# Kernel optimization log

Hardware: AMD Instinct MI355X
Metric: run time of the kernel (lower is better)

## Reference

```python
import jax, jax.numpy as jnp
import numpy as np

D = 1024
B, S = 4, 4096


def setup_inputs() -> dict:
    key = jax.random.key(0)
    ks = jax.random.split(key, 5)
    scale = 1.0 / np.sqrt(D)  # ~ torch Linear init magnitude
    return {
        "x": jax.random.normal(ks[0], (B, S, D), dtype=jnp.float32),
        "Wa": jax.random.normal(ks[1], (D, D), dtype=jnp.float32) * scale,
        "Wb": jax.random.normal(ks[2], (D, D), dtype=jnp.float32) * scale,
        "Wc": jax.random.normal(ks[3], (D, D), dtype=jnp.float32) * scale,
        "Wd": jax.random.normal(ks[4], (D, D), dtype=jnp.float32) * scale,
    }


def reference(x, Wa, Wb, Wc, Wd):
    # torch nn.Linear(bias=False): y = x @ W.T, W is [out, in]
    A = jax.nn.relu(jnp.einsum("bsd,ed->bse", x, Wa))
    Bm = jax.nn.relu(jnp.einsum("bsd,ed->bse", x, Wb))
    C = jax.nn.relu(jnp.einsum("bsd,ed->bse", x, Wc))
    cmp_matrix = jnp.einsum("bse,bte->bst", A, Bm)  # [B,S,S] unnormalized scores
    out = jnp.einsum("bst,bte->bse", cmp_matrix, C)
    return jax.nn.relu(jnp.einsum("bsd,ed->bse", out, Wd))
```

## Files before the change

### kernel.cpp

```cpp
#include <hip/hip_runtime.h>
#include <hip/hip_bf16.h>

#define D_ 1024
#define B_ 4
#define S_ 4096

typedef __attribute__((ext_vector_type(8))) short bf16x8;
typedef __attribute__((ext_vector_type(4))) float f32x4;
typedef __attribute__((ext_vector_type(4))) unsigned int u32x4;
typedef __attribute__((ext_vector_type(4))) unsigned short u16x4;

__device__ __forceinline__ unsigned short f2bf(float f) {
    unsigned int u = __builtin_bit_cast(unsigned int, f);
    u = u + 0x7fffu + ((u >> 16) & 1u);
    return (unsigned short)(u >> 16);
}
__device__ __forceinline__ unsigned int pk2(float a, float b) {
    return (unsigned int)f2bf(a) | ((unsigned int)f2bf(b) << 16);
}
__device__ __forceinline__ float bf2f(unsigned short h) {
    unsigned int u = ((unsigned int)h) << 16;
    return __builtin_bit_cast(float, u);
}
__device__ __forceinline__ void gload16(const void* g, void* l) {
    __builtin_amdgcn_global_load_lds(
        (const __attribute__((address_space(1))) void*)g,
        (__attribute__((address_space(3))) void*)l, 16, 0, 0);
}

__global__ __launch_bounds__(256)
void conv_bf16(const float* __restrict__ src, unsigned short* __restrict__ dst, int n8) {
    int i = blockIdx.x * blockDim.x + threadIdx.x;
    const int stride = gridDim.x * blockDim.x;
    for (; i < n8; i += stride) {
        f32x4 v0 = *(const f32x4*)(src + (size_t)i * 8);
        f32x4 v1 = *(const f32x4*)(src + (size_t)i * 8 + 4);
        u32x4 o;
        o[0] = pk2(v0[0], v0[1]);
        o[1] = pk2(v0[2], v0[3]);
        o[2] = pk2(v1[0], v1[1]);
        o[3] = pk2(v1[2], v1[3]);
        *(u32x4*)(dst + (size_t)i * 8) = o;
    }
}

__global__ __launch_bounds__(256)
void conv_bf16_w4(const float* __restrict__ s0, const float* __restrict__ s1,
                  const float* __restrict__ s2, const float* __restrict__ s3,
                  unsigned short* __restrict__ d0, unsigned short* __restrict__ d1,
                  unsigned short* __restrict__ d2, unsigned short* __restrict__ d3,
                  int n8_per) {
    int i = blockIdx.x * blockDim.x + threadIdx.x;
    const int stride = gridDim.x * blockDim.x;
    for (; i < 4 * n8_per; i += stride) {
        int w = i / n8_per;
        size_t j = (size_t)(i - w * n8_per) * 8;
        const float* s = (w == 0) ? s0 : (w == 1) ? s1 : (w == 2) ? s2 : s3;
        unsigned short* d = (w == 0) ? d0 : (w == 1) ? d1 : (w == 2) ? d2 : d3;
        f32x4 v0 = *(const f32x4*)(s + j);
        f32x4 v1 = *(const f32x4*)(s + j + 4);
        u32x4 o;
        o[0] = pk2(v0[0], v0[1]);
        o[1] = pk2(v0[2], v0[3]);
        o[2] = pk2(v1[0], v1[1]);
        o[3] = pk2(v1[2], v1[3]);
        *(u32x4*)(d + j) = o;
    }
}

__global__ __launch_bounds__(256)
void reduceN_bf16(const unsigned short* __restrict__ P, unsigned short* __restrict__ E,
                  int split, int n8_total) {
    int t = blockIdx.x * blockDim.x + threadIdx.x;
    const int stride = gridDim.x * blockDim.x;
    const int DD = D_ * D_;
    for (; t < n8_total; t += stride) {
        size_t idx = (size_t)t * 8;
        int b = (int)(idx / DD);
        size_t i = idx % DD;
        float s[8];
#pragma unroll
        for (int k = 0; k < 8; ++k) s[k] = 0.f;
        for (int seg = 0; seg < split; ++seg) {
            const unsigned short* p = P + (size_t)(b * split + seg) * DD + i;
            u16x4 v0 = *(const u16x4*)p;
            u16x4 v1 = *(const u16x4*)(p + 4);
#pragma unroll
            for (int k = 0; k < 4; ++k) { s[k] += bf2f(v0[k]); s[4 + k] += bf2f(v1[k]); }
        }
        u16x4 o0, o1;
#pragma unroll
        for (int k = 0; k < 4; ++k) { o0[k] = f2bf(s[k]); o1[k] = f2bf(s[4 + k]); }
        *(u16x4*)(E + idx) = o0;
        *(u16x4*)(E + idx + 4) = o1;
    }
}

#define BM 128
#define BN 128
#define BK 64
#define NTHR 256

template<bool OUT_F32, bool TRANS, bool RELU>
__global__ __launch_bounds__(NTHR)
void gemm_nt(const unsigned short* __restrict__ Ap, const unsigned short* __restrict__ Bp,
             void* __restrict__ Op, int M, int N, int K, int klen, int split,
             long long sA, long long sB, long long sO)
{
    __shared__ char lds_a[BM * BK * 2];
    __shared__ char lds_b[BN * BK * 2];

    const int tid   = threadIdx.x;
    const int bz    = blockIdx.z;
    const int batch = bz / split;
    const int k0    = (bz % split) * klen;
    const int bm    = blockIdx.y * BM;
    const int bn    = blockIdx.x * BN;

    const unsigned short* Abase = Ap + (size_t)batch * sA + (size_t)bm * K;
    const unsigned short* Bbase = Bp + (size_t)batch * sB + (size_t)bn * K;

    const int lane = tid & 63;
    const int wave = tid >> 6;
    const int wm   = (wave >> 1) * 64;
    const int wn   = (wave & 1) * 64;
    const int l16  = lane & 15;
    const int lhi  = lane >> 4;

    const int srow0 = wave * 32 + (lane >> 3);
    const int schnk = (lane & 7) ^ (lane >> 3);
    const char* gA0 = (const char*)(Abase + (size_t)srow0 * K) + schnk * 16;
    const char* gB0 = (const char*)(Bbase + (size_t)srow0 * K) + schnk * 16;
    char* lA0 = lds_a + wave * 4096;
    char* lB0 = lds_b + wave * 4096;

    f32x4 acc[4][4];
#pragma unroll
    for (int i = 0; i < 4; ++i)
#pragma unroll
        for (int j = 0; j < 4; ++j)
            acc[i][j] = (f32x4){0.f, 0.f, 0.f, 0.f};

    for (int kt = k0; kt < k0 + klen; kt += BK) {
#pragma unroll
        for (int p = 0; p < 4; ++p)
            gload16(gA0 + ((size_t)p * 8 * K + kt) * 2, lA0 + p * 1024);
#pragma unroll
        for (int p = 0; p < 4; ++p)
            gload16(gB0 + ((size_t)p * 8 * K + kt) * 2, lB0 + p * 1024);
        __syncthreads();
#pragma unroll
        for (int kk = 0; kk < BK / 32; ++kk) {
            bf16x8 af[4], bfr[4];
#pragma unroll
            for (int i = 0; i < 4; ++i) {
                int row = wm + i * 16 + l16;
                int byt = (row * 128 + kk * 64 + lhi * 16) ^ ((row & 7) << 4);
                af[i] = *(const bf16x8*)(lds_a + byt);
            }
#pragma unroll
            for (int j = 0; j < 4; ++j) {
                int row = wn + j * 16 + l16;
                int byt = (row * 128 + kk * 64 + lhi * 16) ^ ((row & 7) << 4);
                bfr[j] = *(const bf16x8*)(lds_b + byt);
            }
#pragma unroll
            for (int i = 0; i < 4; ++i)
#pragma unroll
                for (int j = 0; j < 4; ++j)
                    acc[i][j] = __builtin_amdgcn_mfma_f32_16x16x32_bf16(af[i], bfr[j], acc[i][j], 0, 0, 0);
        }
        __syncthreads();
    }

    const size_t obase = (size_t)bz * (size_t)sO;
    if constexpr (!TRANS) {
#pragma unroll
        for (int i = 0; i < 4; ++i) {
            const int m0 = bm + wm + i * 16 + lhi * 4;
#pragma unroll
            for (int j = 0; j < 4; ++j) {
                const int n = bn + wn + j * 16 + l16;
#pragma unroll
                for (int r = 0; r < 4; ++r) {
                    float v = acc[i][j][r];
                    if constexpr (RELU) v = fmaxf(v, 0.f);
                    size_t addr = obase + (size_t)(m0 + r) * N + n;
                    if constexpr (OUT_F32) ((float*)Op)[addr] = v;
                    else ((unsigned short*)Op)[addr] = f2bf(v);
                }
            }
        }
    } else {
#pragma unroll
        for (int i = 0; i < 4; ++i) {
            const int m0 = bm + wm + i * 16 + lhi * 4;
#pragma unroll
            for (int j = 0; j < 4; ++j) {
                const int n = bn + wn + j * 16 + l16;
                u16x4 h;
#pragma unroll
                for (int r = 0; r < 4; ++r) {
                    float v = acc[i][j][r];
                    if constexpr (RELU) v = fmaxf(v, 0.f);
                    h[r] = f2bf(v);
                }
                *(u16x4*)((unsigned short*)Op + obase + (size_t)n * M + m0) = h;
            }
        }
    }
}

#define CTILE 65536
#define CBOFF 32768

template<bool OUT_F32, bool TRANS, bool RELU>
__global__ __launch_bounds__(512, 2)
void gemm256(const unsigned short* __restrict__ Ap, const unsigned short* __restrict__ Bp,
             void* __restrict__ Op, int M, int N, int K, int klen, int split,
             long long sA, long long sB, long long sO)
{
    __shared__ char lds[131072];
    const int tid  = threadIdx.x;
    const int wave = tid >> 6;
    const int lane = tid & 63;

    const int gx = gridDim.x, gy = gridDim.y;
    const int f   = blockIdx.x + gx * (blockIdx.y + gy * blockIdx.z);
    const int nwg = gx * gy * (int)gridDim.z;
    const int s   = (f & 7) * (nwg >> 3) + (f >> 3);
    const int lx  = s % gx;
    const int lyz = s / gx;
    const int ly  = lyz % gy;
    const int lz  = lyz / gy;

    const int batch = lz / split;
    const int k0    = (lz % split) * klen;
    const int bm    = ly * 256;
    const int bn    = lx * 256;

    const int wm  = (wave >> 2) * 128;
    const int wn  = (wave & 3) * 64;
    const int l16 = lane & 15, lhi = lane >> 4;

    const unsigned short* Abase = Ap + (size_t)batch * sA + (size_t)bm * K;
    const unsigned short* Bbase = Bp + (size_t)batch * sB + (size_t)bn * K;
    const int srow  = lane >> 3;
    const int schnk = (lane & 7) ^ srow;
    const size_t K2 = (size_t)K * 2;
    const char* gA = (const char*)Abase + (size_t)srow * K2 + (size_t)schnk * 16 + (size_t)k0 * 2;
    const char* gB = (const char*)Bbase + (size_t)srow * K2 + (size_t)schnk * 16 + (size_t)k0 * 2;

    f32x4 acc[8][4];
#pragma unroll
    for (int i = 0; i < 8; ++i)
#pragma unroll
        for (int j = 0; j < 4; ++j)
            acc[i][j] = (f32x4){0.f, 0.f, 0.f, 0.f};

    bf16x8 a[4][2], b0[2][2], b1[2][2];

    auto stageA = [&](int c, int t) {
#pragma unroll
        for (int h = 0; h < 2; ++h)
#pragma unroll
            for (int p = 0; p < 2; ++p)
                gload16(gA + (size_t)t * 128 + (size_t)(h * 128 + wave * 16 + p * 8) * K2,
                        lds + c * CTILE + h * 16384 + wave * 2048 + p * 1024);
    };
    auto stageB = [&](int c, int t) {
#pragma unroll
        for (int h = 0; h < 2; ++h)
#pragma unroll
            for (int p = 0; p < 2; ++p)
                gload16(gB + (size_t)t * 128 + (size_t)(h * 128 + wave * 16 + p * 8) * K2,
                        lds + c * CTILE + CBOFF + h * 16384 + wave * 2048 + p * 1024);
    };
    auto ldA = [&](int c, int mh) {
#pragma unroll
        for (int i4 = 0; i4 < 4; ++i4)
#pragma unroll
            for (int kk = 0; kk < 2; ++kk) {
                int row = wm + mh * 64 + i4 * 16 + l16;
                int byt = (row * 128 + kk * 64 + lhi * 16) ^ ((row & 7) << 4);
                a[i4][kk] = *(const bf16x8*)(lds + c * CTILE + byt);
            }
    };
    auto ldB = [&](int c, int nh, bf16x8 (&bb)[2][2]) {
#pragma unroll
        for (int j2 = 0; j2 < 2; ++j2)
#pragma unroll
            for (int kk = 0; kk < 2; ++kk) {
                int row = wn + nh * 32 + j2 * 16 + l16;
                int byt = (row * 128 + kk * 64 + lhi * 16) ^ ((row & 7) << 4);
                bb[j2][kk] = *(const bf16x8*)(lds + c * CTILE + CBOFF + byt);
            }
    };
    auto mm = [&](int mh, int nh, bf16x8 (&bb)[2][2]) {
        __builtin_amdgcn_s_setprio(1);
#pragma unroll
        for (int i4 = 0; i4 < 4; ++i4)
#pragma unroll
            for (int j2 = 0; j2 < 2; ++j2)
#pragma unroll
                for (int kk = 0; kk < 2; ++kk)
                    acc[mh * 4 + i4][nh * 2 + j2] = __builtin_amdgcn_mfma_f32_16x16x32_bf16(
                        a[i4][kk], bb[j2][kk], acc[mh * 4 + i4][nh * 2 + j2], 0, 0, 0);
        __builtin_amdgcn_s_setprio(0);
    };

#define BAR()  __builtin_amdgcn_s_barrier()
#define LGKM0() asm volatile("s_waitcnt lgkmcnt(0)" ::: "memory")
#define VM4()  asm volatile("s_waitcnt vmcnt(4)" ::: "memory")

    const int NT = klen / 64;
    stageA(0, 0); stageB(0, 0); stageA(1, 1);
    VM4();
    BAR();

    for (int itr = 0; itr < NT / 2; ++itr) {
        const int t1  = 2 * itr + 1;
        const int tp0 = (2 * itr + 2) % NT;
        const int tp1 = (2 * itr + 3) % NT;
        ldA(0, 0); ldB(0, 0, b0); stageB(1, t1);
        BAR(); LGKM0(); mm(0, 0, b0); BAR();
        ldB(0, 1, b1);
        BAR(); LGKM0(); mm(0, 1, b1); BAR();
        ldA(0, 1);
        BAR(); LGKM0(); mm(1, 0, b0); BAR();
        stageA(0, tp0);
        BAR(); mm(1, 1, b1); VM4(); BAR();
        ldA(1, 0); ldB(1, 0, b0); stageB(0, tp0);
        BAR(); LGKM0(); mm(0, 0, b0); BAR();
        ldB(1, 1, b1);
        BAR(); LGKM0(); mm(0, 1, b1); BAR();
        ldA(1, 1);
        BAR(); LGKM0(); mm(1, 0, b0); BAR();
        stageA(1, tp1);
        BAR(); mm(1, 1, b1); VM4(); BAR();
    }
    asm volatile("s_waitcnt vmcnt(0)" ::: "memory");

    const size_t obase = (size_t)lz * (size_t)sO;
    if constexpr (!TRANS) {
#pragma unroll
        for (int i = 0; i < 8; ++i) {
            const int m0 = bm + wm + i * 16 + lhi * 4;
#pragma unroll
            for (int j = 0; j < 4; ++j) {
                const int n = bn + wn + j * 16 + l16;
#pragma unroll
                for (int r = 0; r < 4; ++r) {
                    float v = acc[i][j][r];
                    if constexpr (RELU) v = fmaxf(v, 0.f);
                    size_t addr = obase + (size_t)(m0 + r) * N + n;
                    if constexpr (OUT_F32) ((float*)Op)[addr] = v;
                    else ((unsigned short*)Op)[addr] = f2bf(v);
                }
            }
        }
    } else {
#pragma unroll
        for (int i = 0; i < 8; ++i) {
            const int m0 = bm + wm + i * 16 + lhi * 4;
#pragma unroll
            for (int j = 0; j < 4; ++j) {
                const int n = bn + wn + j * 16 + l16;
                u16x4 h;
#pragma unroll
                for (int r = 0; r < 4; ++r) {
                    float v = acc[i][j][r];
                    if constexpr (RELU) v = fmaxf(v, 0.f);
                    h[r] = f2bf(v);
                }
                *(u16x4*)((unsigned short*)Op + obase + (size_t)n * M + m0) = h;
            }
        }
    }
#undef BAR
#undef LGKM0
#undef VM4
}

extern "C" void kernel_launch(void* const* d_in, const int* in_sizes, int n_in,
                              void* d_out, int out_size, void* d_ws, size_t ws_size,
                              hipStream_t stream) {
    (void)in_sizes; (void)n_in; (void)out_size;
    const float* x  = (const float*)d_in[0];
    const float* Wa = (const float*)d_in[1];
    const float* Wb = (const float*)d_in[2];
    const float* Wc = (const float*)d_in[3];
    const float* Wd = (const float*)d_in[4];

    const long long SD  = (long long)S_ * D_;
    const long long DD2 = (long long)D_ * D_;
    const size_t MB = 1024 * 1024;

    unsigned short* r0 = (unsigned short*)d_ws;
    unsigned short* r1 = (unsigned short*)((char*)d_ws + 32 * MB);
    unsigned short* Ft = r1;
    const bool big_ws = ws_size >= (size_t)96 * MB;

    char* ob = (char*)d_out;
    unsigned short* xb    = (unsigned short*)ob;
    unsigned short* Pp    = big_ws ? (unsigned short*)((char*)d_ws + 64 * MB)
                                   : (unsigned short*)(ob + 32 * MB);
    unsigned short* Enorm = (unsigned short*)(ob + 48 * MB);
    unsigned short* Wbb   = (unsigned short*)(ob + 56 * MB);
    unsigned short* Wcb   = (unsigned short*)(ob + 58 * MB);
    unsigned short* Wab   = (unsigned short*)(ob + 60 * MB);
    unsigned short* Wdb   = (unsigned short*)(ob + 62 * MB);
    const int esplit = big_ws ? 4 : 2;
    const int eklen  = S_ / esplit;

    dim3 blk256(256, 1, 1);
    dim3 blk512(512, 1, 1);
    dim3 gS(D_ / 256, S_ / 256, B_);
    dim3 gE(D_ / 256, D_ / 256, B_ * esplit);
    dim3 gF(D_ / BN, D_ / BM, B_);

    conv_bf16<<<2048, blk256, 0, stream>>>(x, xb, (B_ * S_ * D_) / 8);
    conv_bf16_w4<<<1024, blk256, 0, stream>>>(Wb, Wc, Wa, Wd, Wbb, Wcb, Wab, Wdb, (D_ * D_) / 8);

    gemm256<false, true,  true ><<<gS, blk512, 0, stream>>>(xb, Wbb, r0, S_, D_, D_, D_, 1, SD, 0, SD);
    gemm256<false, true,  true ><<<gS, blk512, 0, stream>>>(xb, Wcb, r1, S_, D_, D_, D_, 1, SD, 0, SD);
    gemm256<false, false, false><<<gE, blk512, 0, stream>>>(r0, r1, Pp, D_, D_, S_, eklen, esplit, SD, SD, DD2);
    reduceN_bf16<<<2048, blk256, 0, stream>>>(Pp, Enorm, esplit, (B_ * D_ * D_) / 8);
    gemm_nt<false, true,  false><<<gF, blk256, 0, stream>>>(Enorm, Wdb, Ft, D_, D_, D_, D_, 1, DD2, 0, DD2);
    gemm256<false, false, true ><<<gS, blk512, 0, stream>>>(xb, Wab, r0, S_, D_, D_, D_, 1, SD, 0, SD);
    gemm256<true,  false, true ><<<gS, blk512, 0, stream>>>(r0, Ft, (float*)d_out, S_, D_, D_, D_, 1, SD, DD2, SD);
}
```

Before: 250.5 us.

## Fuse B/C projections into one GEMM, reduce in place, simplify gemm256 pipeline

The two x@Wb and x@Wc projections become one N=2048 GEMM writing an interleaved buffer. The Gram product reads strided halves of that buffer. The split-K reduction now writes in place over the first partial, and the weight conversions are split and reordered so the out/workspace buffers can be reused. The gemm256 main loop drops the fine-grained half-tile interleaving and instead loads full A/B fragments and issues all MFMAs per K-tile, which needs more registers and may expose more latency. Split-K is fixed at 4 regardless of workspace size, with partials placed in the output buffer.

```diff
diff --git a/kernel.cpp b/kernel.cpp
--- a/kernel.cpp
+++ b/kernel.cpp
@@ -45,18 +45,16 @@
 }
 
 __global__ __launch_bounds__(256)
-void conv_bf16_w4(const float* __restrict__ s0, const float* __restrict__ s1,
-                  const float* __restrict__ s2, const float* __restrict__ s3,
+void conv_bf16_w2(const float* __restrict__ s0, const float* __restrict__ s1,
                   unsigned short* __restrict__ d0, unsigned short* __restrict__ d1,
-                  unsigned short* __restrict__ d2, unsigned short* __restrict__ d3,
                   int n8_per) {
     int i = blockIdx.x * blockDim.x + threadIdx.x;
     const int stride = gridDim.x * blockDim.x;
-    for (; i < 4 * n8_per; i += stride) {
+    for (; i < 2 * n8_per; i += stride) {
         int w = i / n8_per;
         size_t j = (size_t)(i - w * n8_per) * 8;
-        const float* s = (w == 0) ? s0 : (w == 1) ? s1 : (w == 2) ? s2 : s3;
-        unsigned short* d = (w == 0) ? d0 : (w == 1) ? d1 : (w == 2) ? d2 : d3;
+        const float* s = w ? s1 : s0;
+        unsigned short* d = w ? d1 : d0;
         f32x4 v0 = *(const f32x4*)(s + j);
         f32x4 v1 = *(const f32x4*)(s + j + 4);
         u32x4 o;
@@ -69,8 +67,7 @@
 }
 
 __global__ __launch_bounds__(256)
-void reduceN_bf16(const unsigned short* __restrict__ P, unsigned short* __restrict__ E,
-                  int split, int n8_total) {
+void reduceN_bf16_inplace(unsigned short* __restrict__ P, int split, int n8_total) {
     int t = blockIdx.x * blockDim.x + threadIdx.x;
     const int stride = gridDim.x * blockDim.x;
     const int DD = D_ * D_;
@@ -91,8 +88,9 @@
         u16x4 o0, o1;
 #pragma unroll
         for (int k = 0; k < 4; ++k) { o0[k] = f2bf(s[k]); o1[k] = f2bf(s[4 + k]); }
-        *(u16x4*)(E + idx) = o0;
-        *(u16x4*)(E + idx + 4) = o1;
+        unsigned short* e = P + (size_t)(b * split) * DD + i;
+        *(u16x4*)e = o0;
+        *(u16x4*)(e + 4) = o1;
     }
 }
 
@@ -258,86 +256,68 @@
         for (int j = 0; j < 4; ++j)
             acc[i][j] = (f32x4){0.f, 0.f, 0.f, 0.f};
 
-    bf16x8 a[4][2], b0[2][2], b1[2][2];
-
-    auto stageA = [&](int c, int t) {
+    bf16x8 af[8][2], bfr[4][2];
+
+    auto stageAB = [&](int c, int t) {
 #pragma unroll
         for (int h = 0; h < 2; ++h)
 #pragma unroll
-            for (int p = 0; p < 2; ++p)
+            for (int p = 0; p < 2; ++p) {
                 gload16(gA + (size_t)t * 128 + (size_t)(h * 128 + wave * 16 + p * 8) * K2,
                         lds + c * CTILE + h * 16384 + wave * 2048 + p * 1024);
-    };
-    auto stageB = [&](int c, int t) {
-#pragma unroll
-        for (int h = 0; h < 2; ++h)
-#pragma unroll
-            for (int p = 0; p < 2; ++p)
                 gload16(gB + (size_t)t * 128 + (size_t)(h * 128 + wave * 16 + p * 8) * K2,
                         lds + c * CTILE + CBOFF + h * 16384 + wave * 2048 + p * 1024);
+            }
     };
-    auto ldA = [&](int c, int mh) {
-#pragma unroll
-        for (int i4 = 0; i4 < 4; ++i4)
+    auto ldall = [&](int c) {
+#pragma unroll
+        for (int j2 = 0; j2 < 4; ++j2)
 #pragma unroll
             for (int kk = 0; kk < 2; ++kk) {
-                int row = wm + mh * 64 + i4 * 16 + l16;
+                int row = wn + j2 * 16 + l16;
                 int byt = (row * 128 + kk * 64 + lhi * 16) ^ ((row & 7) << 4);
-                a[i4][kk] = *(const bf16x8*)(lds + c * CTILE + byt);
+                bfr[j2][kk] = *(const bf16x8*)(lds + c * CTILE + CBOFF + byt);
+            }
+#pragma unroll
+        for (int i4 = 0; i4 < 8; ++i4)
+#pragma unroll
+            for (int kk = 0; kk < 2; ++kk) {
+                int row = wm + i4 * 16 + l16;
+                int byt = (row * 128 + kk * 64 + lhi * 16) ^ ((row & 7) << 4);
+                af[i4][kk] = *(const bf16x8*)(lds + c * CTILE + byt);
             }
     };
-    auto ldB = [&](int c, int nh, bf16x8 (&bb)[2][2]) {
-#pragma unroll
-        for (int j2 = 0; j2 < 2; ++j2)
-#pragma unroll
-            for (int kk = 0; kk < 2; ++kk) {
-                int row = wn + nh * 32 + j2 * 16 + l16;
-                int byt = (row * 128 + kk * 64 + lhi * 16) ^ ((row & 7) << 4);
-                bb[j2][kk] = *(const bf16x8*)(lds + c * CTILE + CBOFF + byt);
-            }
-    };
-    auto mm = [&](int mh, int nh, bf16x8 (&bb)[2][2]) {
+    auto mmall = [&]() {
         __builtin_amdgcn_s_setprio(1);
 #pragma unroll
-        for (int i4 = 0; i4 < 4; ++i4)
-#pragma unroll
-            for (int j2 = 0; j2 < 2; ++j2)
+        for (int i4 = 0; i4 < 8; ++i4)
+#pragma unroll
+            for (int j2 = 0; j2 < 4; ++j2)
 #pragma unroll
                 for (int kk = 0; kk < 2; ++kk)
-                    acc[mh * 4 + i4][nh * 2 + j2] = __builtin_amdgcn_mfma_f32_16x16x32_bf16(
-                        a[i4][kk], bb[j2][kk], acc[mh * 4 + i4][nh * 2 + j2], 0, 0, 0);
+                    acc[i4][j2] = __builtin_amdgcn_mfma_f32_16x16x32_bf16(
+                        af[i4][kk], bfr[j2][kk], acc[i4][j2], 0, 0, 0);
         __builtin_amdgcn_s_setprio(0);
     };
 
-#define BAR()  __builtin_amdgcn_s_barrier()
+#define BAR()   __builtin_amdgcn_s_barrier()
 #define LGKM0() asm volatile("s_waitcnt lgkmcnt(0)" ::: "memory")
-#define VM4()  asm volatile("s_waitcnt vmcnt(4)" ::: "memory")
+#define VM8()   asm volatile("s_waitcnt vmcnt(8)" ::: "memory")
 
     const int NT = klen / 64;
-    stageA(0, 0); stageB(0, 0); stageA(1, 1);
-    VM4();
+    stageAB(0, 0); stageAB(1, 1);
+    VM8();
     BAR();
 
     for (int itr = 0; itr < NT / 2; ++itr) {
-        const int t1  = 2 * itr + 1;
-        const int tp0 = (2 * itr + 2) % NT;
-        const int tp1 = (2 * itr + 3) % NT;
-        ldA(0, 0); ldB(0, 0, b0); stageB(1, t1);
-        BAR(); LGKM0(); mm(0, 0, b0); BAR();
-        ldB(0, 1, b1);
-        BAR(); LGKM0(); mm(0, 1, b1); BAR();
-        ldA(0, 1);
-        BAR(); LGKM0(); mm(1, 0, b0); BAR();
-        stageA(0, tp0);
-        BAR(); mm(1, 1, b1); VM4(); BAR();
-        ldA(1, 0); ldB(1, 0, b0); stageB(0, tp0);
-        BAR(); LGKM0(); mm(0, 0, b0); BAR();
-        ldB(1, 1, b1);
-        BAR(); LGKM0(); mm(0, 1, b1); BAR();
-        ldA(1, 1);
-        BAR(); LGKM0(); mm(1, 0, b0); BAR();
-        stageA(1, tp1);
-        BAR(); mm(1, 1, b1); VM4(); BAR();
+        ldall(0); mmall();
+        LGKM0(); BAR();
+        stageAB(0, (2 * itr + 2) % NT);
+        VM8(); BAR();
+        ldall(1); mmall();
+        LGKM0(); BAR();
+        stageAB(1, (2 * itr + 3) % NT);
+        VM8(); BAR();
     }
     asm volatile("s_waitcnt vmcnt(0)" ::: "memory");
 
@@ -379,13 +359,13 @@
     }
 #undef BAR
 #undef LGKM0
-#undef VM4
+#undef VM8
 }
 
 extern "C" void kernel_launch(void* const* d_in, const int* in_sizes, int n_in,
                               void* d_out, int out_size, void* d_ws, size_t ws_size,
                               hipStream_t stream) {
-    (void)in_sizes; (void)n_in; (void)out_size;
+    (void)in_sizes; (void)n_in; (void)out_size; (void)ws_size;
     const float* x  = (const float*)d_in[0];
     const float* Wa = (const float*)d_in[1];
     const float* Wb = (const float*)d_in[2];
@@ -396,37 +376,32 @@
     const long long DD2 = (long long)D_ * D_;
     const size_t MB = 1024 * 1024;
 
-    unsigned short* r0 = (unsigned short*)d_ws;
-    unsigned short* r1 = (unsigned short*)((char*)d_ws + 32 * MB);
-    unsigned short* Ft = r1;
-    const bool big_ws = ws_size >= (size_t)96 * MB;
-
+    unsigned short* BC  = (unsigned short*)d_ws;
+    unsigned short* Ao  = (unsigned short*)d_ws;
+    unsigned short* Ft  = (unsigned short*)((char*)d_ws + 32 * MB);
     char* ob = (char*)d_out;
     unsigned short* xb    = (unsigned short*)ob;
-    unsigned short* Pp    = big_ws ? (unsigned short*)((char*)d_ws + 64 * MB)
-                                   : (unsigned short*)(ob + 32 * MB);
-    unsigned short* Enorm = (unsigned short*)(ob + 48 * MB);
+    unsigned short* Pp    = (unsigned short*)(ob + 32 * MB);
+    unsigned short* Enorm = Pp;
+    unsigned short* Wdb   = (unsigned short*)(ob + 34 * MB);
+    unsigned short* Wab   = (unsigned short*)(ob + 36 * MB);
     unsigned short* Wbb   = (unsigned short*)(ob + 56 * MB);
     unsigned short* Wcb   = (unsigned short*)(ob + 58 * MB);
-    unsigned short* Wab   = (unsigned short*)(ob + 60 * MB);
-    unsigned short* Wdb   = (unsigned short*)(ob + 62 * MB);
-    const int esplit = big_ws ? 4 : 2;
-    const int eklen  = S_ / esplit;
 
     dim3 blk256(256, 1, 1);
     dim3 blk512(512, 1, 1);
+    dim3 gBC(2048 / 256, S_ / 256, B_);
+    dim3 gE(D_ / 256, D_ / 256, B_ * 4);
     dim3 gS(D_ / 256, S_ / 256, B_);
-    dim3 gE(D_ / 256, D_ / 256, B_ * esplit);
     dim3 gF(D_ / BN, D_ / BM, B_);
 
     conv_bf16<<<2048, blk256, 0, stream>>>(x, xb, (B_ * S_ * D_) / 8);
-    conv_bf16_w4<<<1024, blk256, 0, stream>>>(Wb, Wc, Wa, Wd, Wbb, Wcb, Wab, Wdb, (D_ * D_) / 8);
-
-    gemm256<false, true,  true ><<<gS, blk512, 0, stream>>>(xb, Wbb, r0, S_, D_, D_, D_, 1, SD, 0, SD);
-    gemm256<false, true,  true ><<<gS, blk512, 0, stream>>>(xb, Wcb, r1, S_, D_, D_, D_, 1, SD, 0, SD);
-    gemm256<false, false, false><<<gE, blk512, 0, stream>>>(r0, r1, Pp, D_, D_, S_, eklen, esplit, SD, SD, DD2);
-    reduceN_bf16<<<2048, blk256, 0, stream>>>(Pp, Enorm, esplit, (B_ * D_ * D_) / 8);
-    gemm_nt<false, true,  false><<<gF, blk256, 0, stream>>>(Enorm, Wdb, Ft, D_, D_, D_, D_, 1, DD2, 0, DD2);
-    gemm256<false, false, true ><<<gS, blk512, 0, stream>>>(xb, Wab, r0, S_, D_, D_, D_, 1, SD, 0, SD);
-    gemm256<true,  false, true ><<<gS, blk512, 0, stream>>>(r0, Ft, (float*)d_out, S_, D_, D_, D_, 1, SD, DD2, SD);
-}
+    conv_bf16_w2<<<512, blk256, 0, stream>>>(Wb, Wc, Wbb, Wcb, (D_ * D_) / 8);
+    gemm256<false, true,  true ><<<gBC, blk512, 0, stream>>>(xb, Wbb, BC, S_, 2048, D_, D_, 1, SD, 0, 2 * SD);
+    gemm256<false, false, false><<<gE, blk512, 0, stream>>>(BC, BC + SD, Pp, D_, D_, S_, S_ / 4, 4, 2 * SD, 2 * SD, DD2);
+    reduceN_bf16_inplace<<<2048, blk256, 0, stream>>>(Pp, 4, (B_ * D_ * D_) / 8);
+    conv_bf16_w2<<<512, blk256, 0, stream>>>(Wd, Wa, Wdb, Wab, (D_ * D_) / 8);
+    gemm_nt<false, true,  false><<<gF, blk256, 0, stream>>>(Enorm, Wdb, Ft, D_, D_, D_, D_, 1, 4 * DD2, 0, DD2);
+    gemm256<false, false, true ><<<gS, blk512, 0, stream>>>(xb, Wab, Ao, S_, D_, D_, D_, 1, SD, 0, SD);
+    gemm256<true,  false, true ><<<gS, blk512, 0, stream>>>(Ao, Ft, (float*)d_out, S_, D_, D_, D_, 1, SD, DD2, SD);
+}
```

New measurement: 323.0 us. 28.9% more time.

## Double-buffer A fragments and prefetch LDS reads ahead of MFMA in GEMM loop

Applied to the files above, without the earlier changes.

Splits the A register fragments into two buffers so LDS reads for the next sub-tile can be issued before the current MFMA block, and removes the explicit lgkmcnt(0) waits. Global staging is reordered: both B chunks are preloaded up front and stageB/stageA are issued at different points with vmcnt(8)/vmcnt(4) waits. The aim is to hide LDS and global latency behind matrix-core work. In exchange it raises register pressure, and correctness now relies on the compiler inserting the LDS waits that were removed.

```diff
diff --git a/kernel.cpp b/kernel.cpp
--- a/kernel.cpp
+++ b/kernel.cpp
@@ -258,7 +258,7 @@
         for (int j = 0; j < 4; ++j)
             acc[i][j] = (f32x4){0.f, 0.f, 0.f, 0.f};
 
-    bf16x8 a[4][2], b0[2][2], b1[2][2];
+    bf16x8 a1[4][2], a2[4][2], b0[2][2], b1[2][2];
 
     auto stageA = [&](int c, int t) {
 #pragma unroll
@@ -276,27 +276,27 @@
                 gload16(gB + (size_t)t * 128 + (size_t)(h * 128 + wave * 16 + p * 8) * K2,
                         lds + c * CTILE + CBOFF + h * 16384 + wave * 2048 + p * 1024);
     };
-    auto ldA = [&](int c, int mh) {
+    auto ldAh = [&](int c, int mh, bf16x8 (&dst)[4][2]) {
 #pragma unroll
         for (int i4 = 0; i4 < 4; ++i4)
 #pragma unroll
             for (int kk = 0; kk < 2; ++kk) {
                 int row = wm + mh * 64 + i4 * 16 + l16;
                 int byt = (row * 128 + kk * 64 + lhi * 16) ^ ((row & 7) << 4);
-                a[i4][kk] = *(const bf16x8*)(lds + c * CTILE + byt);
+                dst[i4][kk] = *(const bf16x8*)(lds + c * CTILE + byt);
             }
     };
-    auto ldB = [&](int c, int nh, bf16x8 (&bb)[2][2]) {
+    auto ldBh = [&](int c, int nh, bf16x8 (&dst)[2][2]) {
 #pragma unroll
         for (int j2 = 0; j2 < 2; ++j2)
 #pragma unroll
             for (int kk = 0; kk < 2; ++kk) {
                 int row = wn + nh * 32 + j2 * 16 + l16;
                 int byt = (row * 128 + kk * 64 + lhi * 16) ^ ((row & 7) << 4);
-                bb[j2][kk] = *(const bf16x8*)(lds + c * CTILE + CBOFF + byt);
+                dst[j2][kk] = *(const bf16x8*)(lds + c * CTILE + CBOFF + byt);
             }
     };
-    auto mm = [&](int mh, int nh, bf16x8 (&bb)[2][2]) {
+    auto mm = [&](int mh, int nh, bf16x8 (&aS)[4][2], bf16x8 (&bS)[2][2]) {
         __builtin_amdgcn_s_setprio(1);
 #pragma unroll
         for (int i4 = 0; i4 < 4; ++i4)
@@ -305,39 +305,46 @@
 #pragma unroll
                 for (int kk = 0; kk < 2; ++kk)
                     acc[mh * 4 + i4][nh * 2 + j2] = __builtin_amdgcn_mfma_f32_16x16x32_bf16(
-                        a[i4][kk], bb[j2][kk], acc[mh * 4 + i4][nh * 2 + j2], 0, 0, 0);
+                        aS[i4][kk], bS[j2][kk], acc[mh * 4 + i4][nh * 2 + j2], 0, 0, 0);
         __builtin_amdgcn_s_setprio(0);
     };
 
 #define BAR()  __builtin_amdgcn_s_barrier()
-#define LGKM0() asm volatile("s_waitcnt lgkmcnt(0)" ::: "memory")
 #define VM4()  asm volatile("s_waitcnt vmcnt(4)" ::: "memory")
-
-    const int NT = klen / 64;
-    stageA(0, 0); stageB(0, 0); stageA(1, 1);
-    VM4();
+#define VM8()  asm volatile("s_waitcnt vmcnt(8)" ::: "memory")
+
+    const int NT  = klen / 64;
+    const int NI  = NT / 2;
+    stageA(0, 0); stageB(0, 0); stageA(1, 1); stageB(1, 1);
+    VM8();
     BAR();
-
-    for (int itr = 0; itr < NT / 2; ++itr) {
-        const int t1  = 2 * itr + 1;
+    ldAh(0, 0, a1); ldBh(0, 0, b0);
+
+    for (int itr = 0; itr < NI; ++itr) {
         const int tp0 = (2 * itr + 2) % NT;
         const int tp1 = (2 * itr + 3) % NT;
-        ldA(0, 0); ldB(0, 0, b0); stageB(1, t1);
-        BAR(); LGKM0(); mm(0, 0, b0); BAR();
-        ldB(0, 1, b1);
-        BAR(); LGKM0(); mm(0, 1, b1); BAR();
-        ldA(0, 1);
-        BAR(); LGKM0(); mm(1, 0, b0); BAR();
-        stageA(0, tp0);
-        BAR(); mm(1, 1, b1); VM4(); BAR();
-        ldA(1, 0); ldB(1, 0, b0); stageB(0, tp0);
-        BAR(); LGKM0(); mm(0, 0, b0); BAR();
-        ldB(1, 1, b1);
-        BAR(); LGKM0(); mm(0, 1, b1); BAR();
-        ldA(1, 1);
-        BAR(); LGKM0(); mm(1, 0, b0); BAR();
-        stageA(1, tp1);
-        BAR(); mm(1, 1, b1); VM4(); BAR();
+        ldBh(0, 1, b1);
+        BAR(); mm(0, 0, a1, b0); BAR();
+        ldAh(0, 1, a2);
+        BAR(); mm(0, 1, a1, b1); BAR();
+        stageB(0, tp0);
+        BAR(); mm(1, 0, a2, b0); BAR();
+        VM4(); stageA(0, tp0);
+        BAR();
+        ldAh(1, 0, a1); ldBh(1, 0, b0);
+        mm(1, 1, a2, b1);
+        BAR();
+        ldBh(1, 1, b1);
+        BAR(); mm(0, 0, a1, b0); BAR();
+        ldAh(1, 1, a2);
+        BAR(); mm(0, 1, a1, b1); BAR();
+        stageB(1, tp1);
+        BAR(); mm(1, 0, a2, b0); BAR();
+        VM4(); stageA(1, tp1);
+        BAR();
+        if (itr + 1 < NI) { ldAh(0, 0, a1); ldBh(0, 0, b0); }
+        mm(1, 1, a2, b1);
+        BAR();
     }
     asm volatile("s_waitcnt vmcnt(0)" ::: "memory");
 
@@ -378,8 +385,8 @@
         }
     }
 #undef BAR
-#undef LGKM0
 #undef VM4
+#undef VM8
 }
 
 extern "C" void kernel_launch(void* const* d_in, const int* in_sizes, int n_in,
```

Result: slower. 500.1 us (+99.6%).
